# Kernel optimization log

Measured on AMD Instinct MI355X. Metric: run time of the kernel, lower is better.

## Reference

```python
import jax, jax.numpy as jnp
import numpy as np


def setup_inputs() -> dict:
    key = jax.random.key(0)
    k1, k2, k3, k4 = jax.random.split(key, 4)
    B, T, I, H = 64, 512, 256, 512
    stdv = 1.0 / np.sqrt(H)
    x = jax.random.normal(k1, (B, T, I), dtype=jnp.float32)
    weight_ih = jax.random.uniform(k2, (I, 4 * H), dtype=jnp.float32, minval=-stdv, maxval=stdv)
    weight_hh = jax.random.uniform(k3, (H, 4 * H), dtype=jnp.float32, minval=-stdv, maxval=stdv)
    bias_ih = jax.random.uniform(k4, (4 * H,), dtype=jnp.float32, minval=-stdv, maxval=stdv)
    return {"x": x, "weight_ih": weight_ih, "weight_hh": weight_hh, "bias_ih": bias_ih}


def reference(x, weight_ih, weight_hh, bias_ih):
    B, T, I = x.shape
    H = weight_hh.shape[0]
    # Precompute input projections for all timesteps: [T, B, 4H]
    x_proj = jnp.einsum('bti,ig->tbg', x, weight_ih) + bias_ih

    def step(carry, xp):
        h, c = carry
        gates = xp + h @ weight_hh  # [B, 4H]
        ig, fg, cg, og = jnp.split(gates, 4, axis=1)
        ig = jax.nn.sigmoid(ig)
        fg = jax.nn.sigmoid(fg)
        cg = jnp.tanh(cg)
        # NOTE: original code applies NO sigmoid to outgate and adds it:
        # hy = outgate * tanh(cy) + outgate
        cy = fg * c + ig * cg
        hy = og * jnp.tanh(cy) + og
        return (hy, cy), hy

    h0 = jnp.zeros((B, H), dtype=x.dtype)
    c0 = jnp.zeros((B, H), dtype=x.dtype)
    _, hs = jax.lax.scan(step, (h0, c0), x_proj)  # hs: [T, B, H]
    return jnp.transpose(hs, (1, 0, 2))  # [B, T, H]
```

## Files before the change

kernel.cpp:

```cpp
#include <hip/hip_runtime.h>
#include <hip/hip_bf16.h>
#include <math.h>

#define BB 64
#define TT 512
#define II 256
#define HH 512
#define GG 2048
#define NBLK 128
#define KP  520
#define XPAD 264

typedef unsigned char u8;
typedef unsigned short u16;
typedef unsigned int u32;
typedef unsigned long long u64;
typedef __attribute__((ext_vector_type(4))) int   i32x4;
typedef __attribute__((ext_vector_type(2))) int   i32x2;
typedef __attribute__((ext_vector_type(4))) short short4v;
typedef __attribute__((ext_vector_type(8))) short short8v;
typedef __attribute__((ext_vector_type(4))) float f32x4;

__device__ __forceinline__ u16 f2bf(float f) {
    unsigned u = __float_as_uint(f);
    unsigned r = (u + 0x7fff + ((u >> 16) & 1)) >> 16;
    return (u16)r;
}
__device__ __forceinline__ float bf2f(u16 h) {
    return __uint_as_float(((unsigned)h) << 16);
}
__device__ __forceinline__ float sigf(float v) {
    return 1.f / (1.f + __expf(-v));
}
__device__ __forceinline__ float tanh_s(float v) {
    float a = fabsf(v);
    float e = __expf(2.f * a);
    float r = 1.f - 2.f / (e + 1.f);
    return copysignf(r, v);
}

#define HLD(dst, base, OFF) \
    asm volatile("global_load_dwordx4 %0, %1, off offset:" OFF " sc0 sc1" \
                 : "=v"(dst) : "v"(base))
#define XLD(dst, voff, sbase) \
    asm volatile("global_load_dwordx4 %0, %1, %2" \
                 : "=v"(dst) : "v"(voff), "s"(sbase))
#define CVTPK(d, lo, hi) \
    asm("v_cvt_pk_bf16_f32 %0, %1, %2" : "=v"(d) : "v"(lo), "v"(hi))

__global__ void __launch_bounds__(64, 1) slstm_kernel(
    const float* __restrict__ x, const float* __restrict__ wih,
    const float* __restrict__ whh, const float* __restrict__ bias,
    float* __restrict__ out, u8* __restrict__ flagb,
    u16* __restrict__ hbuf )
{
    __shared__ u16 lds_whh[4 * 16 * KP];
    __shared__ u16 lds_wih[64 * XPAD];
    __shared__ u16 lds_x[16 * XPAD];

    const int l  = threadIdx.x;
    const int bt = blockIdx.x & 3;
    const int js = blockIdx.x >> 2;
    const int b0 = bt * 16, j0 = js * 16;
    const int c  = l & 15, kq = l >> 4;

    for (int q = 0; q < 4; ++q)
        for (int kk = 0; kk < 128; ++kk) {
            int k = kk * 4 + kq;
            lds_whh[(q * 16 + c) * KP + k] =
                f2bf(whh[(size_t)k * GG + q * 512 + j0 + c]);
        }
    for (int q = 0; q < 4; ++q)
        for (int kk = 0; kk < 64; ++kk) {
            int k = kk * 4 + kq;
            lds_wih[(q * 16 + c) * XPAD + k] =
                f2bf(wih[(size_t)k * GG + q * 512 + j0 + c]);
        }

    float bq[4];
#pragma unroll
    for (int q = 0; q < 4; ++q) bq[q] = bias[q * 512 + j0 + c];

    float cst[4] = {0.f, 0.f, 0.f, 0.f};
    __syncthreads();

    const u32 vbase = (u32)(b0 * TT * II * 4) + 16 * (u32)l;

    f32x4 xr[16];
#pragma unroll
    for (int r = 0; r < 16; ++r) {
        u32 vo = vbase + (u32)(r * TT * II * 4);
        XLD(xr[r], vo, x);
    }
    asm volatile("s_waitcnt vmcnt(0)" ::: "memory");
    __builtin_amdgcn_sched_barrier(0);
#pragma unroll
    for (int r = 0; r < 16; ++r) {
        i32x2 p;
        CVTPK(p[0], xr[r][0], xr[r][1]);
        CVTPK(p[1], xr[r][2], xr[r][3]);
        *(i32x2*)&lds_x[r * XPAD + 4 * l] = p;
    }

    for (int t = 0; t < TT; ++t) {
        i32x4 w0, w1;
        const u8* fb = flagb;
        if (t > 0) {
            fb = flagb + ((size_t)(bt * TT + (t - 1))) * 32;
            asm volatile(
                "global_load_dwordx4 %0, %2, off sc0 sc1\n\t"
                "global_load_dwordx4 %1, %2, off offset:16 sc0 sc1"
                : "=v"(w0), "=v"(w1) : "v"(fb) : "memory");
        }

        const int tn = (t + 1 < TT) ? t + 1 : TT - 1;
#pragma unroll
        for (int r = 0; r < 16; ++r) {
            u32 vo = vbase + (u32)(r * TT * II * 4) + (u32)(tn * II * 4);
            XLD(xr[r], vo, x);
        }

        f32x4 acc[4];
#pragma unroll
        for (int q = 0; q < 4; ++q) acc[q] = (f32x4){bq[q], bq[q], bq[q], bq[q]};
#pragma unroll
        for (int s = 0; s < 8; ++s) {
            short8v a = *(const short8v*)&lds_x[c * XPAD + 32 * s + 8 * kq];
#pragma unroll
            for (int q = 0; q < 4; ++q) {
                short8v b = *(const short8v*)&lds_wih[(q * 16 + c) * XPAD + 32 * s + 8 * kq];
                acc[q] = __builtin_amdgcn_mfma_f32_16x16x32_bf16(a, b, acc[q], 0, 0, 0);
            }
        }

        if (t > 0) {
            asm volatile("s_waitcnt vmcnt(16)" ::: "memory");
            __builtin_amdgcn_sched_barrier(0);
            int m = w0[0] & w0[1] & w0[2] & w0[3] & w1[0] & w1[1] & w1[2] & w1[3];
            while (m != 0x01010101) {
                __builtin_amdgcn_s_sleep(1);
                asm volatile(
                    "global_load_dwordx4 %0, %2, off sc0 sc1\n\t"
                    "global_load_dwordx4 %1, %2, off offset:16 sc0 sc1\n\t"
                    "s_waitcnt vmcnt(0)"
                    : "=v"(w0), "=v"(w1) : "v"(fb) : "memory");
                m = w0[0] & w0[1] & w0[2] & w0[3] & w1[0] & w1[1] & w1[2] & w1[3];
            }
            __builtin_amdgcn_sched_barrier(0);
        }

        const int rp = (t - 1) & 1;
        const u16* hb = hbuf + (size_t)(rp * 2) * BB * HH + (size_t)(b0 + c) * HH + 8 * kq;
        const u16* lb = hb + BB * HH;
        i32x4 h0,h1,h2,h3,h4,h5,h6,h7,h8,h9,h10,h11,h12,h13,h14,h15;
        i32x4 g0,g1,g2,g3,g4,g5,g6,g7,g8,g9,g10,g11,g12,g13,g14,g15;
        HLD(h0, hb,   "0"); HLD(g0, lb,   "0");
        HLD(h1, hb,  "64"); HLD(g1, lb,  "64");
        HLD(h2, hb, "128"); HLD(g2, lb, "128");
        HLD(h3, hb, "192"); HLD(g3, lb, "192");
        HLD(h4, hb, "256"); HLD(g4, lb, "256");
        HLD(h5, hb, "320"); HLD(g5, lb, "320");
        HLD(h6, hb, "384"); HLD(g6, lb, "384");
        HLD(h7, hb, "448"); HLD(g7, lb, "448");
        HLD(h8, hb, "512"); HLD(g8, lb, "512");
        HLD(h9, hb, "576"); HLD(g9, lb, "576");
        HLD(h10,hb, "640"); HLD(g10,lb, "640");
        HLD(h11,hb, "704"); HLD(g11,lb, "704");
        HLD(h12,hb, "768"); HLD(g12,lb, "768");
        HLD(h13,hb, "832"); HLD(g13,lb, "832");
        HLD(h14,hb, "896"); HLD(g14,lb, "896");
        HLD(h15,hb, "960"); HLD(g15,lb, "960");

#define HMM(S, FH, FL) do {                                                     \
        short8v ah_ = __builtin_bit_cast(short8v, FH);                          \
        short8v al_ = __builtin_bit_cast(short8v, FL);                          \
        _Pragma("unroll")                                                       \
        for (int q = 0; q < 4; ++q) {                                           \
            short8v b_ = *(const short8v*)&lds_whh[(q * 16 + c) * KP + 32 * (S) + 8 * kq]; \
            acc[q] = __builtin_amdgcn_mfma_f32_16x16x32_bf16(ah_, b_, acc[q], 0, 0, 0); \
            acc[q] = __builtin_amdgcn_mfma_f32_16x16x32_bf16(al_, b_, acc[q], 0, 0, 0); \
        }                                                                       \
    } while (0)

        asm volatile("s_waitcnt vmcnt(16)" ::: "memory");
        __builtin_amdgcn_sched_barrier(0);
        HMM(0, h0, g0); HMM(1, h1, g1); HMM(2, h2, g2); HMM(3, h3, g3);
        HMM(4, h4, g4); HMM(5, h5, g5); HMM(6, h6, g6); HMM(7, h7, g7);
        asm volatile("s_waitcnt vmcnt(0)" ::: "memory");
        __builtin_amdgcn_sched_barrier(0);
        HMM(8, h8, g8); HMM(9, h9, g9); HMM(10,h10,g10); HMM(11,h11,g11);
        HMM(12,h12,g12); HMM(13,h13,g13); HMM(14,h14,g14); HMM(15,h15,g15);

        const int wp = t & 1;
        u16* hdst_hi = hbuf + (size_t)(wp * 2) * BB * HH;
        u16* hdst_lo = hdst_hi + BB * HH;
        const int j = j0 + c;
#pragma unroll
        for (int rg = 0; rg < 4; ++rg) {
            int b = b0 + kq * 4 + rg;
            float ig = sigf(acc[0][rg]);
            float fg = sigf(acc[1][rg]);
            float cg = tanh_s(acc[2][rg]);
            float og = acc[3][rg];
            float cy = fg * cst[rg] + ig * cg;
            cst[rg] = cy;
            float hy = og * tanh_s(cy) + og;
            out[((size_t)b * TT + t) * HH + j] = hy;
            u16 hi = f2bf(hy);
            float lo = hy - bf2f(hi);
            __hip_atomic_store(&hdst_hi[(size_t)b * HH + j], hi,
                               __ATOMIC_RELAXED, __HIP_MEMORY_SCOPE_AGENT);
            __hip_atomic_store(&hdst_lo[(size_t)b * HH + j], f2bf(lo),
                               __ATOMIC_RELAXED, __HIP_MEMORY_SCOPE_AGENT);
        }

#pragma unroll
        for (int r = 0; r < 16; ++r) {
            i32x2 p;
            CVTPK(p[0], xr[r][0], xr[r][1]);
            CVTPK(p[1], xr[r][2], xr[r][3]);
            *(i32x2*)&lds_x[r * XPAD + 4 * l] = p;
        }

        asm volatile("s_waitcnt vmcnt(0)" ::: "memory");
        if (l == 0)
            __hip_atomic_store(flagb + ((size_t)(bt * TT + t)) * 32 + js, (u8)1,
                               __ATOMIC_RELAXED, __HIP_MEMORY_SCOPE_AGENT);
    }
}

extern "C" void kernel_launch(void* const* d_in, const int* in_sizes, int n_in,
                              void* d_out, int out_size, void* d_ws, size_t ws_size,
                              hipStream_t stream) {
    const float* x    = (const float*)d_in[0];
    const float* wih  = (const float*)d_in[1];
    const float* whh  = (const float*)d_in[2];
    const float* bias = (const float*)d_in[3];
    float* out = (float*)d_out;

    u8*  flagb = (u8*)d_ws;
    u16* hbuf  = (u16*)((char*)d_ws + 65536);
    size_t clear = 65536 + (size_t)2 * 2 * BB * HH * sizeof(u16);
    hipMemsetAsync(d_ws, 0, clear, stream);

    hipLaunchKernelGGL(slstm_kernel, dim3(NBLK), dim3(64), 0, stream,
                       x, wih, whh, bias, out, flagb, hbuf);
}
```

Before: 2.549 ms.

## Reorder LSTM step loop to shorten the cross-block critical path

Restructures the per-timestep loop so the input-projection MFMAs for step t+1 run after the flag is published, moving them off the inter-block dependency chain. The flag is now signalled before the output store, and the wait is split into two halves so the first half of h can be loaded and used while the second half's producers are still finishing. The memset of the h buffer is dropped because step 0 no longer reads it. The waitcnt counts are adjusted to the new load order, which is fragile if the issue order changes.

```diff
diff --git a/kernel.cpp b/kernel.cpp
--- a/kernel.cpp
+++ b/kernel.cpp
@@ -14,10 +14,8 @@
 typedef unsigned char u8;
 typedef unsigned short u16;
 typedef unsigned int u32;
-typedef unsigned long long u64;
 typedef __attribute__((ext_vector_type(4))) int   i32x4;
 typedef __attribute__((ext_vector_type(2))) int   i32x2;
-typedef __attribute__((ext_vector_type(4))) short short4v;
 typedef __attribute__((ext_vector_type(8))) short short8v;
 typedef __attribute__((ext_vector_type(4))) float f32x4;
 
@@ -80,7 +78,6 @@
     float bq[4];
 #pragma unroll
     for (int q = 0; q < 4; ++q) bq[q] = bias[q * 512 + j0 + c];
-
     float cst[4] = {0.f, 0.f, 0.f, 0.f};
     __syncthreads();
 
@@ -101,75 +98,18 @@
         CVTPK(p[1], xr[r][2], xr[r][3]);
         *(i32x2*)&lds_x[r * XPAD + 4 * l] = p;
     }
-
-    for (int t = 0; t < TT; ++t) {
-        i32x4 w0, w1;
-        const u8* fb = flagb;
-        if (t > 0) {
-            fb = flagb + ((size_t)(bt * TT + (t - 1))) * 32;
-            asm volatile(
-                "global_load_dwordx4 %0, %2, off sc0 sc1\n\t"
-                "global_load_dwordx4 %1, %2, off offset:16 sc0 sc1"
-                : "=v"(w0), "=v"(w1) : "v"(fb) : "memory");
-        }
-
-        const int tn = (t + 1 < TT) ? t + 1 : TT - 1;
-#pragma unroll
-        for (int r = 0; r < 16; ++r) {
-            u32 vo = vbase + (u32)(r * TT * II * 4) + (u32)(tn * II * 4);
-            XLD(xr[r], vo, x);
-        }
-
-        f32x4 acc[4];
-#pragma unroll
-        for (int q = 0; q < 4; ++q) acc[q] = (f32x4){bq[q], bq[q], bq[q], bq[q]};
-#pragma unroll
-        for (int s = 0; s < 8; ++s) {
-            short8v a = *(const short8v*)&lds_x[c * XPAD + 32 * s + 8 * kq];
-#pragma unroll
-            for (int q = 0; q < 4; ++q) {
-                short8v b = *(const short8v*)&lds_wih[(q * 16 + c) * XPAD + 32 * s + 8 * kq];
-                acc[q] = __builtin_amdgcn_mfma_f32_16x16x32_bf16(a, b, acc[q], 0, 0, 0);
-            }
-        }
-
-        if (t > 0) {
-            asm volatile("s_waitcnt vmcnt(16)" ::: "memory");
-            __builtin_amdgcn_sched_barrier(0);
-            int m = w0[0] & w0[1] & w0[2] & w0[3] & w1[0] & w1[1] & w1[2] & w1[3];
-            while (m != 0x01010101) {
-                __builtin_amdgcn_s_sleep(1);
-                asm volatile(
-                    "global_load_dwordx4 %0, %2, off sc0 sc1\n\t"
-                    "global_load_dwordx4 %1, %2, off offset:16 sc0 sc1\n\t"
-                    "s_waitcnt vmcnt(0)"
-                    : "=v"(w0), "=v"(w1) : "v"(fb) : "memory");
-                m = w0[0] & w0[1] & w0[2] & w0[3] & w1[0] & w1[1] & w1[2] & w1[3];
-            }
-            __builtin_amdgcn_sched_barrier(0);
-        }
-
-        const int rp = (t - 1) & 1;
-        const u16* hb = hbuf + (size_t)(rp * 2) * BB * HH + (size_t)(b0 + c) * HH + 8 * kq;
-        const u16* lb = hb + BB * HH;
-        i32x4 h0,h1,h2,h3,h4,h5,h6,h7,h8,h9,h10,h11,h12,h13,h14,h15;
-        i32x4 g0,g1,g2,g3,g4,g5,g6,g7,g8,g9,g10,g11,g12,g13,g14,g15;
-        HLD(h0, hb,   "0"); HLD(g0, lb,   "0");
-        HLD(h1, hb,  "64"); HLD(g1, lb,  "64");
-        HLD(h2, hb, "128"); HLD(g2, lb, "128");
-        HLD(h3, hb, "192"); HLD(g3, lb, "192");
-        HLD(h4, hb, "256"); HLD(g4, lb, "256");
-        HLD(h5, hb, "320"); HLD(g5, lb, "320");
-        HLD(h6, hb, "384"); HLD(g6, lb, "384");
-        HLD(h7, hb, "448"); HLD(g7, lb, "448");
-        HLD(h8, hb, "512"); HLD(g8, lb, "512");
-        HLD(h9, hb, "576"); HLD(g9, lb, "576");
-        HLD(h10,hb, "640"); HLD(g10,lb, "640");
-        HLD(h11,hb, "704"); HLD(g11,lb, "704");
-        HLD(h12,hb, "768"); HLD(g12,lb, "768");
-        HLD(h13,hb, "832"); HLD(g13,lb, "832");
-        HLD(h14,hb, "896"); HLD(g14,lb, "896");
-        HLD(h15,hb, "960"); HLD(g15,lb, "960");
+    f32x4 acc[4];
+#pragma unroll
+    for (int q = 0; q < 4; ++q) acc[q] = (f32x4){bq[q], bq[q], bq[q], bq[q]};
+#pragma unroll
+    for (int s = 0; s < 8; ++s) {
+        short8v a = *(const short8v*)&lds_x[c * XPAD + 32 * s + 8 * kq];
+#pragma unroll
+        for (int q = 0; q < 4; ++q) {
+            short8v b = *(const short8v*)&lds_wih[(q * 16 + c) * XPAD + 32 * s + 8 * kq];
+            acc[q] = __builtin_amdgcn_mfma_f32_16x16x32_bf16(a, b, acc[q], 0, 0, 0);
+        }
+    }
 
 #define HMM(S, FH, FL) do {                                                     \
         short8v ah_ = __builtin_bit_cast(short8v, FH);                          \
@@ -182,19 +122,90 @@
         }                                                                       \
     } while (0)
 
-        asm volatile("s_waitcnt vmcnt(16)" ::: "memory");
-        __builtin_amdgcn_sched_barrier(0);
-        HMM(0, h0, g0); HMM(1, h1, g1); HMM(2, h2, g2); HMM(3, h3, g3);
-        HMM(4, h4, g4); HMM(5, h5, g5); HMM(6, h6, g6); HMM(7, h7, g7);
-        asm volatile("s_waitcnt vmcnt(0)" ::: "memory");
-        __builtin_amdgcn_sched_barrier(0);
-        HMM(8, h8, g8); HMM(9, h9, g9); HMM(10,h10,g10); HMM(11,h11,g11);
-        HMM(12,h12,g12); HMM(13,h13,g13); HMM(14,h14,g14); HMM(15,h15,g15);
+    for (int t = 0; t < TT; ++t) {
+        i32x4 h0,h1,h2,h3,h4,h5,h6,h7,h8,h9,h10,h11,h12,h13,h14,h15;
+        i32x4 g0,g1,g2,g3,g4,g5,g6,g7,g8,g9,g10,g11,g12,g13,g14,g15;
+        const int have_h = (t > 0);
+
+        if (have_h) {
+            const u8* fb = flagb + ((size_t)(bt * TT + (t - 1))) * 32;
+            i32x4 wA, wB;
+            int bReady;
+            while (true) {
+                asm volatile(
+                    "global_load_dwordx4 %0, %2, off sc0 sc1\n\t"
+                    "global_load_dwordx4 %1, %2, off offset:16 sc0 sc1\n\t"
+                    "s_waitcnt vmcnt(0)"
+                    : "=v"(wA), "=v"(wB) : "v"(fb) : "memory");
+                int mA = wA[0] & wA[1] & wA[2] & wA[3];
+                if (mA == 0x01010101) {
+                    int mB = wB[0] & wB[1] & wB[2] & wB[3];
+                    bReady = (mB == 0x01010101);
+                    break;
+                }
+                __builtin_amdgcn_s_sleep(1);
+            }
+            __builtin_amdgcn_sched_barrier(0);
+
+            const int rp = (t - 1) & 1;
+            const u16* hb = hbuf + (size_t)(rp * 2) * BB * HH
+                            + (size_t)(b0 + c) * HH + 8 * kq;
+            const u16* lb = hb + BB * HH;
+            HLD(h0, hb,   "0"); HLD(g0, lb,   "0");
+            HLD(h1, hb,  "64"); HLD(g1, lb,  "64");
+            HLD(h2, hb, "128"); HLD(g2, lb, "128");
+            HLD(h3, hb, "192"); HLD(g3, lb, "192");
+            HLD(h4, hb, "256"); HLD(g4, lb, "256");
+            HLD(h5, hb, "320"); HLD(g5, lb, "320");
+            HLD(h6, hb, "384"); HLD(g6, lb, "384");
+            HLD(h7, hb, "448"); HLD(g7, lb, "448");
+
+            if (!bReady) {
+                while (true) {
+                    asm volatile(
+                        "global_load_dwordx4 %0, %1, off offset:16 sc0 sc1\n\t"
+                        "s_waitcnt vmcnt(0)"
+                        : "=v"(wB) : "v"(fb) : "memory");
+                    int mB = wB[0] & wB[1] & wB[2] & wB[3];
+                    if (mB == 0x01010101) break;
+                    __builtin_amdgcn_s_sleep(1);
+                }
+                __builtin_amdgcn_sched_barrier(0);
+            }
+
+            HLD(h8, hb, "512"); HLD(g8, lb, "512");
+            HLD(h9, hb, "576"); HLD(g9, lb, "576");
+            HLD(h10,hb, "640"); HLD(g10,lb, "640");
+            HLD(h11,hb, "704"); HLD(g11,lb, "704");
+            HLD(h12,hb, "768"); HLD(g12,lb, "768");
+            HLD(h13,hb, "832"); HLD(g13,lb, "832");
+            HLD(h14,hb, "896"); HLD(g14,lb, "896");
+            HLD(h15,hb, "960"); HLD(g15,lb, "960");
+        }
+
+        const int tn = (t + 1 < TT) ? t + 1 : TT - 1;
+#pragma unroll
+        for (int r = 0; r < 16; ++r) {
+            u32 vo = vbase + (u32)(r * TT * II * 4) + (u32)(tn * II * 4);
+            XLD(xr[r], vo, x);
+        }
+
+        if (have_h) {
+            asm volatile("s_waitcnt vmcnt(32)" ::: "memory");
+            __builtin_amdgcn_sched_barrier(0);
+            HMM(0, h0, g0); HMM(1, h1, g1); HMM(2, h2, g2); HMM(3, h3, g3);
+            HMM(4, h4, g4); HMM(5, h5, g5); HMM(6, h6, g6); HMM(7, h7, g7);
+            asm volatile("s_waitcnt vmcnt(16)" ::: "memory");
+            __builtin_amdgcn_sched_barrier(0);
+            HMM(8, h8, g8); HMM(9, h9, g9); HMM(10,h10,g10); HMM(11,h11,g11);
+            HMM(12,h12,g12); HMM(13,h13,g13); HMM(14,h14,g14); HMM(15,h15,g15);
+        }
 
         const int wp = t & 1;
         u16* hdst_hi = hbuf + (size_t)(wp * 2) * BB * HH;
         u16* hdst_lo = hdst_hi + BB * HH;
         const int j = j0 + c;
+        float hyv[4];
 #pragma unroll
         for (int rg = 0; rg < 4; ++rg) {
             int b = b0 + kq * 4 + rg;
@@ -205,7 +216,7 @@
             float cy = fg * cst[rg] + ig * cg;
             cst[rg] = cy;
             float hy = og * tanh_s(cy) + og;
-            out[((size_t)b * TT + t) * HH + j] = hy;
+            hyv[rg] = hy;
             u16 hi = f2bf(hy);
             float lo = hy - bf2f(hi);
             __hip_atomic_store(&hdst_hi[(size_t)b * HH + j], hi,
@@ -214,6 +225,17 @@
                                __ATOMIC_RELAXED, __HIP_MEMORY_SCOPE_AGENT);
         }
 
+        asm volatile("s_waitcnt vmcnt(0)" ::: "memory");
+        if (l == 0)
+            __hip_atomic_store(flagb + ((size_t)(bt * TT + t)) * 32 + js, (u8)1,
+                               __ATOMIC_RELAXED, __HIP_MEMORY_SCOPE_AGENT);
+
+#pragma unroll
+        for (int rg = 0; rg < 4; ++rg) {
+            int b = b0 + kq * 4 + rg;
+            out[((size_t)b * TT + t) * HH + j] = hyv[rg];
+        }
+
 #pragma unroll
         for (int r = 0; r < 16; ++r) {
             i32x2 p;
@@ -222,10 +244,17 @@
             *(i32x2*)&lds_x[r * XPAD + 4 * l] = p;
         }
 
-        asm volatile("s_waitcnt vmcnt(0)" ::: "memory");
-        if (l == 0)
-            __hip_atomic_store(flagb + ((size_t)(bt * TT + t)) * 32 + js, (u8)1,
-                               __ATOMIC_RELAXED, __HIP_MEMORY_SCOPE_AGENT);
+#pragma unroll
+        for (int q = 0; q < 4; ++q) acc[q] = (f32x4){bq[q], bq[q], bq[q], bq[q]};
+#pragma unroll
+        for (int s = 0; s < 8; ++s) {
+            short8v a = *(const short8v*)&lds_x[c * XPAD + 32 * s + 8 * kq];
+#pragma unroll
+            for (int q = 0; q < 4; ++q) {
+                short8v b = *(const short8v*)&lds_wih[(q * 16 + c) * XPAD + 32 * s + 8 * kq];
+                acc[q] = __builtin_amdgcn_mfma_f32_16x16x32_bf16(a, b, acc[q], 0, 0, 0);
+            }
+        }
     }
 }
 
@@ -240,8 +269,7 @@
 
     u8*  flagb = (u8*)d_ws;
     u16* hbuf  = (u16*)((char*)d_ws + 65536);
-    size_t clear = 65536 + (size_t)2 * 2 * BB * HH * sizeof(u16);
-    hipMemsetAsync(d_ws, 0, clear, stream);
+    hipMemsetAsync(d_ws, 0, 65536, stream);
 
     hipLaunchKernelGGL(slstm_kernel, dim3(NBLK), dim3(64), 0, stream,
                        x, wih, whh, bias, out, flagb, hbuf);
```

Measured after the change: 2.710 ms. +6.3%, slower.
